# Kernel tuning notes

Hardware: AMD Instinct MI355X
Metric: run time of the kernel (lower is better)

The kernel has to match this reference:

```python
import jax, jax.numpy as jnp
import numpy as np

B, S, D, H = 8, 512, 1024, 16
DPH = D // H
MAXREL = 16
EDGE_TYPE = 4
NEG = -9e15  # matches torch's -9000000000000000.0 edge mask fill


def setup_inputs() -> dict:
    key = jax.random.key(0)
    ks = jax.random.split(key, 16)
    sd = 0.02
    inp = {
        'key':   jax.random.normal(ks[0], (B, S, D), jnp.float32),
        'value': jax.random.normal(ks[1], (B, S, D), jnp.float32),
        'query': jax.random.normal(ks[2], (B, S, D), jnp.float32),
        'grh':   jax.random.randint(ks[3], (B, S, S), 0, 5, jnp.int32),
        'mask':  jnp.zeros((B, S, S), jnp.bool_),
        # projection weights, stored (in, out)
        'Wq': jax.random.normal(ks[4], (D, D), jnp.float32) * sd,
        'bq': jnp.zeros((D,), jnp.float32),
        'Wk': jax.random.normal(ks[5], (D, D), jnp.float32) * sd,
        'bk': jnp.zeros((D,), jnp.float32),
        'Wv': jax.random.normal(ks[6], (D, D), jnp.float32) * sd,
        'bv': jnp.zeros((D,), jnp.float32),
        # relative position embedding table (vocab = 2*MAXREL+1, dph)
        'rel_emb': jax.random.normal(ks[7], (2 * MAXREL + 1, DPH), jnp.float32) * sd,
        # 2*(edge_type+1) = 10 per-head linears dph -> 1
        'att_w': jax.random.normal(ks[8], (2 * (EDGE_TYPE + 1), DPH), jnp.float32) * sd,
        'att_b': jnp.zeros((2 * (EDGE_TYPE + 1),), jnp.float32),
        # edge_type+2 = 6 gate linears D -> D
        'gate_w': jax.random.normal(ks[9], (EDGE_TYPE + 2, D, D), jnp.float32) * sd,
        'gate_b': jnp.zeros((EDGE_TYPE + 2, D), jnp.float32),
        # sub_final_linear: (D + D*edge_type) -> D
        'sub_w': jax.random.normal(ks[10], (D + D * EDGE_TYPE, D), jnp.float32) * sd,
        'sub_b': jnp.zeros((D,), jnp.float32),
    }
    return inp


def _forward(key, value, query, grh, mask, Wq, bq, Wk, bk, Wv, bv,
             rel_emb, att_w, att_b, gate_w, gate_b, sub_w, sub_b):
    def shape4(x):  # (B,S,D) -> (B,H,S,dph)
        return x.reshape(B, S, H, DPH).transpose(0, 2, 1, 3)

    def unshape(x):  # (B,H,S,dph) -> (B,S,D)
        return x.transpose(0, 2, 1, 3).reshape(B, S, D)

    q = shape4(query @ Wq + bq) / jnp.sqrt(jnp.float32(DPH))
    k = shape4(key @ Wk + bk)
    v = shape4(value @ Wv + bv)

    # relative position bias (attn_type='self', no cache)
    pos = jnp.arange(S)
    rpm = jnp.clip(pos[None, :] - pos[:, None], -MAXREL, MAXREL) + MAXREL  # (S,S)
    rel = rel_emb[rpm]  # (S,S,dph); same table used for keys and values

    scores = jnp.einsum('bhqd,bhkd->bhqk', q, k) + jnp.einsum('bhqd,qkd->bhqk', q, rel)
    scores = jnp.where(mask[:, None], jnp.float32(-1e18), scores)
    attn = jax.nn.softmax(scores, axis=-1)  # dropout p=0 (eval)

    ctx = jnp.einsum('bhqk,bhkd->bhqd', attn, v) + jnp.einsum('bhqk,qkd->bhqd', attn, rel)
    context = unshape(ctx)
    gate_context = jax.nn.sigmoid(context @ gate_w[0] + gate_b[0]) * context

    top_attn = attn[:, 0]  # (B,S,S)

    def edge_view(i0, i1, adj, gi):
        h_i = jnp.einsum('bhsd,d->bhs', v, att_w[i0]) + att_b[i0]  # (B,H,S)
        h_j = jnp.einsum('bhsd,d->bhs', v, att_w[i1]) + att_b[i1]
        e = jax.nn.leaky_relu(h_i[..., :, None] + h_j[..., None, :])  # (B,H,S,S)
        a = jax.nn.softmax(jnp.where(adj[:, None], e, jnp.float32(NEG)), axis=-1)
        sub = unshape(jnp.einsum('bhqk,bhkd->bhqd', a, v))
        return jax.nn.sigmoid(sub @ gate_w[gi] + gate_b[gi]) * sub

    # whole-graph view: adj = grh > 1, uses linear_attention[6],[7], gate_linear[-1]
    views = [edge_view(6, 7, grh > 1, EDGE_TYPE + 1)]
    eye = jnp.eye(S, dtype=grh.dtype)
    for i in range(EDGE_TYPE - 1):
        label = i + 2
        adj = grh == (label + eye * (4 - label))  # diagonal label sums to 4
        views.append(edge_view(2 * i, 2 * i + 1, adj, i + 1))

    out = jnp.concatenate([gate_context] + views, axis=-1) @ sub_w + sub_b
    return out, top_attn


def reference(key, value, query, grh, mask, Wq, bq, Wk, bk, Wv, bv,
              rel_emb, att_w, att_b, gate_w, gate_b, sub_w, sub_b):
    return _forward(key, value, query, grh, mask, Wq, bq, Wk, bk, Wv, bv,
                    rel_emb, att_w, att_b, gate_w, gate_b, sub_w, sub_b)
```

## Files before the change

### kernel.cpp

```cpp
#include <hip/hip_runtime.h>
#include <hip/hip_bf16.h>

typedef __hip_bfloat16 bf16;
typedef __attribute__((ext_vector_type(8))) short bf16x8;
typedef __attribute__((ext_vector_type(4))) float f32x4;

#define B_ 8
#define S_ 512
#define D_ 1024
#define H_ 16
#define NEGV -9.0e15f
#define WSL 1048576ull

__device__ __forceinline__ float bf2f(bf16 x) { return __bfloat162float(x); }
__device__ __forceinline__ float us2f(unsigned short u) {
  union { unsigned int i; float f; } c; c.i = ((unsigned int)u) << 16; return c.f;
}
__device__ __forceinline__ unsigned short f2us(float f) {
  bf16 h = __float2bfloat16(f);
  unsigned short u; __builtin_memcpy(&u, &h, 2); return u;
}
__device__ __forceinline__ float ldx(const void* p, size_t i, int isbf) {
  return isbf ? bf2f(((const bf16*)p)[i]) : ((const float*)p)[i];
}
struct F4 { float x, y, z, w; };
__device__ __forceinline__ F4 ld4(const void* p, size_t i, int isbf) {
  F4 r;
  if (isbf) {
    ushort4 u = *(const ushort4*)((const bf16*)p + i);
    r.x = us2f(u.x); r.y = us2f(u.y); r.z = us2f(u.z); r.w = us2f(u.w);
  } else {
    float4 d = *(const float4*)((const float*)p + i);
    r.x = d.x; r.y = d.y; r.z = d.z; r.w = d.w;
  }
  return r;
}
__device__ __forceinline__ bf16x8 ld8bf(const void* p, size_t i, int isbf) {
  if (isbf) return *(const bf16x8*)((const bf16*)p + i);
  float4 a = *(const float4*)((const float*)p + i);
  float4 b = *(const float4*)((const float*)p + i + 4);
  bf16x8 r;
  r[0] = (short)f2us(a.x); r[1] = (short)f2us(a.y);
  r[2] = (short)f2us(a.z); r[3] = (short)f2us(a.w);
  r[4] = (short)f2us(b.x); r[5] = (short)f2us(b.y);
  r[6] = (short)f2us(b.z); r[7] = (short)f2us(b.w);
  return r;
}
__device__ __forceinline__ f32x4 mfma_bf16(bf16x8 a, bf16x8 b, f32x4 c) {
  return __builtin_amdgcn_mfma_f32_16x16x32_bf16(a, b, c, 0, 0, 0);
}
__device__ __forceinline__ void gload16(const bf16* g, short* l) {
  __builtin_amdgcn_global_load_lds(
      (const __attribute__((address_space(1))) void*)g,
      (__attribute__((address_space(3))) void*)l, 16, 0, 0);
}

__global__ void detect_k(const void* __restrict__ w, int* __restrict__ flag)
{
  if (threadIdx.x == 0 && blockIdx.x == 0) {
    const unsigned short* u = (const unsigned short*)w;
    int sane = 0;
    for (int i = 0; i < 1024; i += 2) {
      float a = fabsf(us2f(u[i]));
      if (a == 0.f || (a > 9.5e-7f && a < 8.f)) sane++;
    }
    *flag = (sane > 256) ? 1 : 0;
  }
}

__global__ __launch_bounds__(256)
void cvt_k(const void* __restrict__ q, const void* __restrict__ k,
           const void* __restrict__ v, bf16* __restrict__ out,
           const int* __restrict__ dflag)
{
  const int isbf = *dflag;
  const int z = blockIdx.y;
  const void* src = z == 0 ? q : (z == 1 ? k : v);
  size_t i = ((size_t)blockIdx.x * 256 + threadIdx.x) * 8;
  bf16x8 r = ld8bf(src, i, isbf);
  *(bf16x8*)(out + (size_t)z * 4194304 + i) = r;
}

__global__ __launch_bounds__(256)
void mask_pack_k(const int* __restrict__ grh, unsigned char* __restrict__ maskp)
{
  int t = blockIdx.x * 256 + threadIdx.x;
  int byte = t & 63, qi = (t >> 6) & 511, bl = t >> 15;
  const int* g = grh + ((size_t)bl * 512 + qi) * 512 + byte * 8;
  int4 a = *(const int4*)g;
  int4 b = *(const int4*)(g + 4);
  int gs[8] = {a.x, a.y, a.z, a.w, b.x, b.y, b.z, b.w};
  unsigned int m0 = 0, m1 = 0, m2 = 0, m3 = 0;
  #pragma unroll
  for (int j = 0; j < 8; j++) {
    int k = byte * 8 + j;
    int diag = (k == qi);
    m0 |= (unsigned int)(gs[j] > 1) << j;
    m1 |= (unsigned int)(gs[j] == (diag ? 4 : 2)) << j;
    m2 |= (unsigned int)(gs[j] == (diag ? 4 : 3)) << j;
    m3 |= (unsigned int)(gs[j] == 4) << j;
  }
  size_t o = (size_t)bl * 32768 + (size_t)qi * 64 + byte;
  maskp[o]          = (unsigned char)m0;
  maskp[o + 262144] = (unsigned char)m1;
  maskp[o + 524288] = (unsigned char)m2;
  maskp[o + 786432] = (unsigned char)m3;
}

__global__ __launch_bounds__(256)
void wtrans_all_k(const void* __restrict__ Wq, const void* __restrict__ Wk,
                  const void* __restrict__ Wv, const void* __restrict__ gate_w,
                  const void* __restrict__ sub_w, bf16* __restrict__ Wt,
                  const int* __restrict__ dflag)
{
  const int isbf = *dflag;
  const int slot = blockIdx.x >> 8;
  const int blk = blockIdx.x & 255;
  const int gsrc[5] = {0, 5, 1, 2, 3};
  const void* W;
  size_t woff;
  if (slot < 3)      { W = slot == 0 ? Wq : (slot == 1 ? Wk : Wv); woff = 0; }
  else if (slot < 8) { W = gate_w; woff = (size_t)gsrc[slot - 3] * WSL; }
  else               { W = sub_w;  woff = (size_t)(slot - 8) * WSL; }
  bf16* out = Wt + (size_t)slot * WSL;

  __shared__ float t[64][68];
  const int tid = threadIdx.x;
  const int nt = blk & 15, kt = blk >> 4;
  {
    int r = tid >> 4, c4 = (tid & 15) * 4;
    #pragma unroll
    for (int i = 0; i < 4; i++) {
      int rr = r + i * 16;
      F4 v = ld4(W, woff + (size_t)(kt * 64 + rr) * 1024 + nt * 64 + c4, isbf);
      *(float4*)&t[rr][c4] = make_float4(v.x, v.y, v.z, v.w);
    }
  }
  __syncthreads();
  {
    int n = tid >> 4, k4 = (tid & 15) * 4;
    #pragma unroll
    for (int i = 0; i < 4; i++) {
      int nn = n + i * 16;
      ushort4 u;
      u.x = f2us(t[k4 + 0][nn]); u.y = f2us(t[k4 + 1][nn]);
      u.z = f2us(t[k4 + 2][nn]); u.w = f2us(t[k4 + 3][nn]);
      *(ushort4*)(out + (size_t)(nt * 64 + nn) * 1024 + kt * 64 + k4) = u;
    }
  }
}

__global__ __launch_bounds__(256)
void qkv_gemm_k(const bf16* __restrict__ qkvb, const bf16* __restrict__ Wt,
                const void* __restrict__ bqp, const void* __restrict__ bkp,
                const void* __restrict__ bvp, bf16* __restrict__ qbf,
                bf16* __restrict__ kbf, bf16* __restrict__ vtb,
                const int* __restrict__ dflag)
{
  const int isbf = *dflag;
  const int z = blockIdx.z;
  const bf16* A = qkvb + (size_t)z * 4194304;
  const void* bias = z == 0 ? bqp : (z == 1 ? bkp : bvp);
  bf16* outB = z == 0 ? qbf : (z == 1 ? kbf : vtb);
  const bf16* Wz = Wt + (size_t)z * WSL;
  const float scale = z == 0 ? 0.125f : 1.0f;
  const int vtrans = (z == 2);

  __shared__ short As[128 * 64];
  __shared__ short Bs[128 * 64];
  const int tid = threadIdx.x;
  const int w = tid >> 6, ln = tid & 63;
  const int ln15 = ln & 15, quad = ln >> 4;
  const int wm = (w & 1) * 64, wn = (w >> 1) * 64;
  const int bm = blockIdx.x * 128, bn = blockIdx.y * 128;
  const int rbase = w * 8 + (ln >> 3);
  const int goff = ((ln & 7) ^ (ln >> 3)) * 8;
  f32x4 acc[4][4];
  #pragma unroll
  for (int mt = 0; mt < 4; mt++)
    #pragma unroll
    for (int nt = 0; nt < 4; nt++) acc[mt][nt] = (f32x4)(0.0f);

  for (int k0 = 0; k0 < 1024; k0 += 64) {
    #pragma unroll
    for (int i = 0; i < 4; i++) {
      int r = i * 32 + rbase;
      gload16(A + (size_t)(bm + r) * 1024 + k0 + goff,
              &As[(i * 32 + w * 8) * 64]);
      gload16(Wz + (size_t)(bn + r) * 1024 + k0 + goff,
              &Bs[(i * 32 + w * 8) * 64]);
    }
    __syncthreads();
    #pragma unroll
    for (int s = 0; s < 2; s++) {
      bf16x8 af[4], bfr[4];
      #pragma unroll
      for (int t = 0; t < 4; t++) {
        int ra = wm + t * 16 + ln15;
        af[t] = *(bf16x8*)&As[ra * 64 + (((s * 4 + quad) ^ (ra & 7)) * 8)];
        int rb = wn + t * 16 + ln15;
        bfr[t] = *(bf16x8*)&Bs[rb * 64 + (((s * 4 + quad) ^ (rb & 7)) * 8)];
      }
      #pragma unroll
      for (int mt = 0; mt < 4; mt++)
        #pragma unroll
        for (int nt = 0; nt < 4; nt++)
          acc[mt][nt] = mfma_bf16(af[mt], bfr[nt], acc[mt][nt]);
    }
    __syncthreads();
  }

  #pragma unroll
  for (int nt = 0; nt < 4; nt++) {
    int col = bn + wn + nt * 16 + ln15;
    float bv = ldx(bias, col, isbf);
    #pragma unroll
    for (int mt = 0; mt < 4; mt++) {
      #pragma unroll
      for (int r = 0; r < 4; r++) {
        int row = bm + wm + mt * 16 + quad * 4 + r;
        float v = (acc[mt][nt][r] + bv) * scale;
        int bb = row >> 9, s = row & 511;
        int h = col >> 6, d0 = col & 63;
        size_t o = vtrans ? (((size_t)(bb * 16 + h) * 64 + d0) * 512 + s)
                          : (((size_t)(bb * 16 + h) * 512 + s) * 64 + d0);
        outB[o] = __float2bfloat16(v);
      }
    }
  }
}

__global__ __launch_bounds__(256)
void gate_gemm_k(const bf16* __restrict__ ctx5, const bf16* __restrict__ Wt,
                 const void* __restrict__ gate_b, bf16* __restrict__ gated5,
                 const int* __restrict__ dflag)
{
  const int isbf = *dflag;
  const int z = blockIdx.z;
  const int gsel[5] = {0, 5, 1, 2, 3};
  const bf16* A = ctx5 + (size_t)z * 4194304;
  bf16* outB = gated5 + (size_t)z * 4194304;
  const bf16* Wz = Wt + (size_t)(3 + z) * WSL;
  const size_t boff = (size_t)gsel[z] * 1024;

  __shared__ short As[128 * 64];
  __shared__ short Bs[128 * 64];
  const int tid = threadIdx.x;
  const int w = tid >> 6, ln = tid & 63;
  const int ln15 = ln & 15, quad = ln >> 4;
  const int wm = (w & 1) * 64, wn = (w >> 1) * 64;
  const int bm = blockIdx.x * 128, bn = blockIdx.y * 128;
  const int rbase = w * 8 + (ln >> 3);
  const int goff = ((ln & 7) ^ (ln >> 3)) * 8;
  f32x4 acc[4][4];
  #pragma unroll
  for (int mt = 0; mt < 4; mt++)
    #pragma unroll
    for (int nt = 0; nt < 4; nt++) acc[mt][nt] = (f32x4)(0.0f);

  for (int k0 = 0; k0 < 1024; k0 += 64) {
    #pragma unroll
    for (int i = 0; i < 4; i++) {
      int r = i * 32 + rbase;
      gload16(A + (size_t)(bm + r) * 1024 + k0 + goff,
              &As[(i * 32 + w * 8) * 64]);
      gload16(Wz + (size_t)(bn + r) * 1024 + k0 + goff,
              &Bs[(i * 32 + w * 8) * 64]);
    }
    __syncthreads();
    #pragma unroll
    for (int s = 0; s < 2; s++) {
      bf16x8 af[4], bfr[4];
      #pragma unroll
      for (int t = 0; t < 4; t++) {
        int ra = wm + t * 16 + ln15;
        af[t] = *(bf16x8*)&As[ra * 64 + (((s * 4 + quad) ^ (ra & 7)) * 8)];
        int rb = wn + t * 16 + ln15;
        bfr[t] = *(bf16x8*)&Bs[rb * 64 + (((s * 4 + quad) ^ (rb & 7)) * 8)];
      }
      #pragma unroll
      for (int mt = 0; mt < 4; mt++)
        #pragma unroll
        for (int nt = 0; nt < 4; nt++)
          acc[mt][nt] = mfma_bf16(af[mt], bfr[nt], acc[mt][nt]);
    }
    __syncthreads();
  }

  #pragma unroll
  for (int nt = 0; nt < 4; nt++) {
    int col = bn + wn + nt * 16 + ln15;
    float bv = ldx(gate_b, boff + col, isbf);
    #pragma unroll
    for (int mt = 0; mt < 4; mt++) {
      #pragma unroll
      for (int r = 0; r < 4; r++) {
        int row = bm + wm + mt * 16 + quad * 4 + r;
        float v = acc[mt][nt][r] + bv;
        float x = bf2f(A[(size_t)row * 1024 + col]);
        outB[(size_t)row * 1024 + col] = __float2bfloat16(x / (1.f + __expf(-v)));
      }
    }
  }
}

__global__ __launch_bounds__(256)
void sub_gemm_k(const bf16* __restrict__ gated5, const bf16* __restrict__ Wt,
                const void* __restrict__ sub_b, void* __restrict__ dout,
                const int* __restrict__ dflag)
{
  const int isbf = *dflag;
  __shared__ short As[128 * 64];
  __shared__ short Bs[128 * 64];
  const int tid = threadIdx.x;
  const int w = tid >> 6, ln = tid & 63;
  const int ln15 = ln & 15, quad = ln >> 4;
  const int wm = (w & 1) * 64, wn = (w >> 1) * 64;
  const int bm = blockIdx.x * 128, bn = blockIdx.y * 128;
  const int rbase = w * 8 + (ln >> 3);
  const int goff = ((ln & 7) ^ (ln >> 3)) * 8;
  f32x4 acc[4][4];
  #pragma unroll
  for (int mt = 0; mt < 4; mt++)
    #pragma unroll
    for (int nt = 0; nt < 4; nt++) acc[mt][nt] = (f32x4)(0.0f);

  for (int k0 = 0; k0 < 5120; k0 += 64) {
    const int slot = k0 >> 10, kk = k0 & 1023;
    const bf16* Ab = gated5 + (size_t)slot * 4194304;
    const bf16* Wz = Wt + (size_t)(8 + slot) * WSL;
    #pragma unroll
    for (int i = 0; i < 4; i++) {
      int r = i * 32 + rbase;
      gload16(Ab + (size_t)(bm + r) * 1024 + kk + goff,
              &As[(i * 32 + w * 8) * 64]);
      gload16(Wz + (size_t)(bn + r) * 1024 + kk + goff,
              &Bs[(i * 32 + w * 8) * 64]);
    }
    __syncthreads();
    #pragma unroll
    for (int s = 0; s < 2; s++) {
      bf16x8 af[4], bfr[4];
      #pragma unroll
      for (int t = 0; t < 4; t++) {
        int ra = wm + t * 16 + ln15;
        af[t] = *(bf16x8*)&As[ra * 64 + (((s * 4 + quad) ^ (ra & 7)) * 8)];
        int rb = wn + t * 16 + ln15;
        bfr[t] = *(bf16x8*)&Bs[rb * 64 + (((s * 4 + quad) ^ (rb & 7)) * 8)];
      }
      #pragma unroll
      for (int mt = 0; mt < 4; mt++)
        #pragma unroll
        for (int nt = 0; nt < 4; nt++)
          acc[mt][nt] = mfma_bf16(af[mt], bfr[nt], acc[mt][nt]);
    }
    __syncthreads();
  }

  #pragma unroll
  for (int nt = 0; nt < 4; nt++) {
    int col = bn + wn + nt * 16 + ln15;
    float bv = ldx(sub_b, col, isbf);
    #pragma unroll
    for (int mt = 0; mt < 4; mt++) {
      #pragma unroll
      for (int r = 0; r < 4; r++) {
        int row = bm + wm + mt * 16 + quad * 4 + r;
        float v = acc[mt][nt][r] + bv;
        size_t o = (size_t)row * 1024 + col;
        if (isbf) ((bf16*)dout)[o] = __float2bfloat16(v);
        else      ((float*)dout)[o] = v;
      }
    }
  }
}

__global__ __launch_bounds__(256)
void qrel_k(const bf16* __restrict__ qbf, const void* __restrict__ rel_emb,
            float* __restrict__ G, const int* __restrict__ dflag)
{
  const int isbf = *dflag;
  __shared__ float rel[33][65];
  __shared__ float qw[4][64];
  const int tid = threadIdx.x;
  for (int i = tid; i < 33 * 64; i += 256)
    rel[i >> 6][i & 63] = ldx(rel_emb, i, isbf);
  const int wv = tid >> 6, lane = tid & 63;
  const size_t row = (size_t)blockIdx.x * 4 + wv;
  qw[wv][lane] = bf2f(qbf[row * 64 + lane]);
  __syncthreads();
  if (lane < 33) {
    float s = 0.f;
    #pragma unroll
    for (int d = 0; d < 64; d++) s += qw[wv][d] * rel[lane][d];
    G[row * 33 + lane] = s;
  }
}

__global__ __launch_bounds__(256, 2)
void score_fused_k(const bf16* __restrict__ qbf, const bf16* __restrict__ kbf,
                   const float* __restrict__ G, const bf16* __restrict__ vt,
                   const void* __restrict__ rel_emb, bf16* __restrict__ ctx,
                   void* __restrict__ dout, const int* __restrict__ dflag)
{
  __shared__ short P[32 * 512];
  __shared__ float gbuf[32 * 33];
  __shared__ float relbuf[33 * 64];
  __shared__ float smax[4][16];
  __shared__ float ssumS[4][16];
  __shared__ float sleS[4][16];
  __shared__ float sgeS[4][16];
  const int tid = threadIdx.x;
  const int w = tid >> 6, ln = tid & 63;
  const int ln15 = ln & 15, quad = ln >> 4;
  const int rowg = (w >> 1) * 16;
  const int ch = w & 1;
  const int bh = blockIdx.x, qt = blockIdx.y;
  const size_t qrow0 = (size_t)bh * 512 + qt * 32;
  const int isbf = *dflag;

  for (int i = tid; i < 32 * 33; i += 256) {
    int r = i / 33, c = i - r * 33;
    gbuf[i] = G[(qrow0 + r) * 33 + c];
  }
  for (int i = tid; i < 33 * 64; i += 256)
    relbuf[i] = ldx(rel_emb, i, isbf);

  const bf16* qrow = qbf + (qrow0 + rowg + ln15) * 64;
  bf16x8 af0 = *(const bf16x8*)(qrow + quad * 8);
  bf16x8 af1 = *(const bf16x8*)(qrow + 32 + quad * 8);
  const bf16* kb = kbf + (size_t)bh * 512 * 64;
  f32x4 acc[16];
  #pragma unroll
  for (int t = 0; t < 16; t++) acc[t] = (f32x4)(0.0f);
  #pragma unroll
  for (int t = 0; t < 16; t++) {
    const bf16* kr = kb + (size_t)(ch * 256 + t * 16 + ln15) * 64 + quad * 8;
    bf16x8 b0 = *(const bf16x8*)kr;
    bf16x8 b1 = *(const bf16x8*)(kr + 32);
    acc[t] = mfma_bf16(af0, b0, acc[t]);
    acc[t] = mfma_bf16(af1, b1, acc[t]);
  }
  __syncthreads();

  const int qg = qt * 32 + rowg + quad * 4;
  const int rowl0 = rowg + quad * 4;
  float mx[4], ssum[4], sle[4], sge[4], inv[4];
  #pragma unroll
  for (int r = 0; r < 4; r++) mx[r] = -3.0e38f;
  #pragma unroll
  for (int t = 0; t < 16; t++) {
    int k = ch * 256 + t * 16 + ln15;
    #pragma unroll
    for (int r = 0; r < 4; r++) {
      int delta = k - (qg + r);
      int bkt = delta < -16 ? 0 : (delta > 16 ? 32 : delta + 16);
      float s = acc[t][r] + gbuf[(rowl0 + r) * 33 + bkt];
      acc[t][r] = s;
      mx[r] = fmaxf(mx[r], s);
    }
  }
  #pragma unroll
  for (int r = 0; r < 4; r++) {
    float m = mx[r];
    #pragma unroll
    for (int off = 1; off < 16; off <<= 1) m = fmaxf(m, __shfl_xor(m, off));
    mx[r] = m;
  }
  if (ln15 == 0) {
    #pragma unroll
    for (int r = 0; r < 4; r++) smax[w][quad * 4 + r] = mx[r];
  }
  __syncthreads();
  #pragma unroll
  for (int r = 0; r < 4; r++) {
    mx[r] = fmaxf(mx[r], smax[w ^ 1][quad * 4 + r]);
    ssum[r] = 0.f; sle[r] = 0.f; sge[r] = 0.f;
  }

  #pragma unroll
  for (int t = 0; t < 16; t++) {
    int k = ch * 256 + t * 16 + ln15;
    #pragma unroll
    for (int r = 0; r < 4; r++) {
      float p = __expf(acc[t][r] - mx[r]);
      acc[t][r] = p;
      ssum[r] += p;
      int delta = k - (qg + r);
      if (delta <= -16) sle[r] += p;
      if (delta >= 16) sge[r] += p;
    }
  }
  #pragma unroll
  for (int r = 0; r < 4; r++) {
    #pragma unroll
    for (int off = 1; off < 16; off <<= 1) {
      ssum[r] += __shfl_xor(ssum[r], off);
      sle[r] += __shfl_xor(sle[r], off);
      sge[r] += __shfl_xor(sge[r], off);
    }
  }
  if (ln15 == 0) {
    #pragma unroll
    for (int r = 0; r < 4; r++) {
      ssumS[w][quad * 4 + r] = ssum[r];
      sleS[w][quad * 4 + r] = sle[r];
      sgeS[w][quad * 4 + r] = sge[r];
    }
  }
  __syncthreads();
  #pragma unroll
  for (int r = 0; r < 4; r++) {
    float tot = ssum[r] + ssumS[w ^ 1][quad * 4 + r];
    sle[r] += sleS[w ^ 1][quad * 4 + r];
    sge[r] += sgeS[w ^ 1][quad * 4 + r];
    inv[r] = 1.f / tot;
  }

  #pragma unroll
  for (int t2 = 0; t2 < 16; t2++) {
    int gg = t2 * 2 + (ln15 >> 3);
    int slot = gg ^ (quad << 1);
    #pragma unroll
    for (int r = 0; r < 4; r++) {
      int rowL = rowl0 + r;
      P[rowL * 512 + ch * 256 + slot * 8 + (ln15 & 7)] =
          (short)f2us(acc[t2][r] * inv[r]);
    }
  }
  __syncthreads();

  if ((bh & 15) == 0) {
    const int bg = bh >> 4;
    for (int i = tid; i < 32 * 64; i += 256) {
      int rowL = i >> 6, g = i & 63;
      int chg = g >> 5, gg = g & 31;
      int slot = gg ^ (((rowL >> 2) & 3) << 1);
      bf16x8 u = *(bf16x8*)&P[rowL * 512 + chg * 256 + slot * 8];
      size_t o = (size_t)4194304 + (size_t)bg * 262144 +
                 (size_t)(qt * 32 + rowL) * 512 + g * 8;
      if (isbf) {
        *(bf16x8*)((bf16*)dout + o) = u;
      } else {
        float4 f0 = make_float4(us2f((unsigned short)u[0]), us2f((unsigned short)u[1]),
                                us2f((unsigned short)u[2]), us2f((unsigned short)u[3]));
        float4 f1 = make_float4(us2f((unsigned short)u[4]), us2f((unsigned short)u[5]),
                                us2f((unsigned short)u[6]), us2f((unsigned short)u[7]));
        *(float4*)((float*)dout + o) = f0;
        *(float4*)((float*)dout + o + 4) = f1;
      }
    }
  }

  const bf16* vb = vt + (size_t)bh * 64 * 512;
  f32x4 pacc[2];
  pacc[0] = (f32x4)(0.0f); pacc[1] = (f32x4)(0.0f);
  const int ra = rowg + ln15;
  const int rsw = ((ln15 >> 2) & 3) << 1;
  #pragma unroll
  for (int h2 = 0; h2 < 2; h2++) {
    #pragma unroll
    for (int kk = 0; kk < 8; kk++) {
      int gg = kk * 4 + quad;
      bf16x8 a = *(bf16x8*)&P[ra * 512 + h2 * 256 + ((gg ^ rsw) * 8)];
      int k0 = h2 * 256 + kk * 32;
      #pragma unroll
      for (int nt2 = 0; nt2 < 2; nt2++) {
        int dcol = ch * 32 + nt2 * 16 + ln15;
        bf16x8 b = *(const bf16x8*)(vb + (size_t)dcol * 512 + k0 + quad * 8);
        pacc[nt2] = mfma_bf16(a, b, pacc[nt2]);
      }
    }
  }

  for (int rr = 1; rr < 32; rr++) {
    float av[4];
    #pragma unroll
    for (int r = 0; r < 4; r++) {
      int k = qg + r + rr - 16;
      av[r] = 0.f;
      if (k >= 0 && k < 512) {
        int g = k >> 3, chg = g >> 5, gg = g & 31;
        int slot = gg ^ (quad << 1);
        av[r] = us2f((unsigned short)P[(rowl0 + r) * 512 + chg * 256 +
                                       slot * 8 + (k & 7)]);
      }
    }
    #pragma unroll
    for (int nt2 = 0; nt2 < 2; nt2++) {
      float relv = relbuf[rr * 64 + ch * 32 + nt2 * 16 + ln15];
      #pragma unroll
      for (int r = 0; r < 4; r++) pacc[nt2][r] += av[r] * relv;
    }
  }

  #pragma unroll
  for (int nt2 = 0; nt2 < 2; nt2++) {
    float r0v = relbuf[ch * 32 + nt2 * 16 + ln15];
    float r32v = relbuf[32 * 64 + ch * 32 + nt2 * 16 + ln15];
    #pragma unroll
    for (int r = 0; r < 4; r++)
      pacc[nt2][r] += sle[r] * inv[r] * r0v + sge[r] * inv[r] * r32v;
  }

  const int bl = bh >> 4, head = bh & 15;
  #pragma unroll
  for (int r = 0; r < 4; r++) {
    int s = qt * 32 + rowl0 + r;
    #pragma unroll
    for (int nt2 = 0; nt2 < 2; nt2++)
      ctx[((size_t)bl * 512 + s) * 1024 + head * 64 + ch * 32 + nt2 * 16 + ln15] =
          __float2bfloat16(pacc[nt2][r]);
  }
}

__global__ __launch_bounds__(256)
void hv_k(const bf16* __restrict__ vt, const void* __restrict__ att_w,
          const void* __restrict__ att_b, float* __restrict__ h0,
          float* __restrict__ h1, const int* __restrict__ dflag)
{
  const int i0s[4] = {6, 0, 2, 4};
  const int i1s[4] = {7, 1, 3, 5};
  const int z = blockIdx.y;
  const int i0 = i0s[z], i1 = i1s[z];
  __shared__ float w0[64], w1[64];
  const int tid = threadIdx.x;
  const int bh = blockIdx.x;
  const int isbf = *dflag;
  if (tid < 64) {
    w0[tid] = ldx(att_w, i0 * 64 + tid, isbf);
    w1[tid] = ldx(att_w, i1 * 64 + tid, isbf);
  }
  __syncthreads();
  const bf16* vb = vt + (size_t)bh * 64 * 512 + tid * 2;
  float a00 = 0, a01 = 0, a10 = 0, a11 = 0;
  for (int d = 0; d < 64; d++) {
    ushort2 u = *(const ushort2*)(vb + (size_t)d * 512);
    float f0 = us2f(u.x), f1 = us2f(u.y);
    a00 += f0 * w0[d]; a10 += f1 * w0[d];
    a01 += f0 * w1[d]; a11 += f1 * w1[d];
  }
  float b0 = ldx(att_b, i0, isbf), b1 = ldx(att_b, i1, isbf);
  float* p0 = h0 + (size_t)z * 65536 + (size_t)bh * 512 + tid * 2;
  float* p1 = h1 + (size_t)z * 65536 + (size_t)bh * 512 + tid * 2;
  p0[0] = a00 + b0; p0[1] = a10 + b0;
  p1[0] = a01 + b1; p1[1] = a11 + b1;
}

__global__ __launch_bounds__(256)
void edge_fused_k(const float* __restrict__ h0, const float* __restrict__ h1,
                  const unsigned char* __restrict__ maskp,
                  const bf16* __restrict__ vt, bf16* __restrict__ ctx5)
{
  __shared__ short P[32 * 512];
  const int tid = threadIdx.x;
  const int w = tid >> 6, ln = tid & 63;
  const int ln15 = ln & 15, quad = ln >> 4;
  const int bh = blockIdx.x, qt = blockIdx.y, view = blockIdx.z;
  const int bl = bh >> 4;
  bf16* ctx = ctx5 + (size_t)(1 + view) * 4194304;

  {
    const float* hjp = h1 + (size_t)view * 65536 + (size_t)bh * 512 + ln * 8;
    float4 hA = *(const float4*)hjp;
    float4 hB = *(const float4*)(hjp + 4);
    float hjv[8] = {hA.x, hA.y, hA.z, hA.w, hB.x, hB.y, hB.z, hB.w};
    const float* h0b = h0 + (size_t)view * 65536 + (size_t)bh * 512 + qt * 32 + w * 8;
    const unsigned char* mrow = maskp + (size_t)view * 262144 + (size_t)bl * 32768
                                + (size_t)(qt * 32 + w * 8) * 64 + ln;
    unsigned int mb[8];
    float hi[8];
    #pragma unroll
    for (int rr = 0; rr < 8; rr++) mb[rr] = mrow[rr * 64];
    #pragma unroll
    for (int rr = 0; rr < 8; rr++) hi[rr] = h0b[rr];

    float e[8][8];
    float mx[8], sm[8];
    #pragma unroll
    for (int rr = 0; rr < 8; rr++) {
      float m = -3.0e38f;
      #pragma unroll
      for (int j = 0; j < 8; j++) {
        float ej = hi[rr] + hjv[j];
        ej = ej >= 0.f ? ej : 0.01f * ej;
        e[rr][j] = ((mb[rr] >> j) & 1) ? ej : NEGV;
        m = fmaxf(m, e[rr][j]);
      }
      mx[rr] = m;
    }
    #pragma unroll
    for (int off = 32; off; off >>= 1) {
      #pragma unroll
      for (int rr = 0; rr < 8; rr++)
        mx[rr] = fmaxf(mx[rr], __shfl_xor(mx[rr], off));
    }
    #pragma unroll
    for (int rr = 0; rr < 8; rr++) {
      float s = 0.f;
      #pragma unroll
      for (int j = 0; j < 8; j++) {
        e[rr][j] = __expf(e[rr][j] - mx[rr]);
        s += e[rr][j];
      }
      sm[rr] = s;
    }
    #pragma unroll
    for (int off = 32; off; off >>= 1) {
      #pragma unroll
      for (int rr = 0; rr < 8; rr++)
        sm[rr] += __shfl_xor(sm[rr], off);
    }
    #pragma unroll
    for (int rr = 0; rr < 8; rr++) {
      float inv = 1.f / sm[rr];
      int r = w * 8 + rr;
      bf16x8 pv;
      #pragma unroll
      for (int j = 0; j < 8; j++) pv[j] = (short)f2us(e[rr][j] * inv);
      *(bf16x8*)&P[r * 512 + ((ln ^ (r & 7)) * 8)] = pv;
    }
  }
  __syncthreads();

  const bf16* vb = vt + (size_t)bh * 64 * 512;
  const int m0 = (w >> 1) * 16, d0 = (w & 1) * 32;
  f32x4 acc[2];
  acc[0] = (f32x4)(0.0f); acc[1] = (f32x4)(0.0f);

  const int ra = m0 + ln15;
  const int rsw = ra & 7;
  #pragma unroll 4
  for (int k0 = 0; k0 < 512; k0 += 32) {
    int gsel = (k0 >> 3) + quad;
    bf16x8 a = *(bf16x8*)&P[ra * 512 + ((gsel ^ rsw) * 8)];
    #pragma unroll
    for (int nt = 0; nt < 2; nt++) {
      bf16x8 b = *(const bf16x8*)(vb + (size_t)(d0 + nt * 16 + ln15) * 512 + k0 + quad * 8);
      acc[nt] = mfma_bf16(a, b, acc[nt]);
    }
  }

  const int head = bh & 15;
  #pragma unroll
  for (int r = 0; r < 4; r++) {
    int s = qt * 32 + m0 + quad * 4 + r;
    #pragma unroll
    for (int nt = 0; nt < 2; nt++)
      ctx[((size_t)bl * 512 + s) * 1024 + head * 64 + d0 + nt * 16 + ln15] =
          __float2bfloat16(acc[nt][r]);
  }
}

extern "C" void kernel_launch(void* const* d_in, const int* in_sizes, int n_in,
                              void* d_out, int out_size, void* d_ws, size_t ws_size,
                              hipStream_t stream)
{
  const void* key   = d_in[0];
  const void* value = d_in[1];
  const void* query = d_in[2];
  const int*  grh   = (const int*)d_in[3];
  const void* Wq = d_in[5];
  const void* bq = d_in[6];
  const void* Wk = d_in[7];
  const void* bk = d_in[8];
  const void* Wv = d_in[9];
  const void* bv = d_in[10];
  const void* rel_emb = d_in[11];
  const void* att_w = d_in[12];
  const void* att_b = d_in[13];
  const void* gate_w = d_in[14];
  const void* gate_b = d_in[15];
  const void* sub_w = d_in[16];
  const void* sub_b = d_in[17];

  int* dflag = (int*)d_ws;
  float* base = (float*)d_ws;
  bf16* qbf = (bf16*)(base + 16);
  bf16* kbf = (bf16*)(base + 16 + 2097152);
  bf16* vtb = (bf16*)(base + 16 + 2 * 2097152);
  bf16* Wt  = (bf16*)(base + 16 + 3 * 2097152);
  float* G  = base + 16 + 3 * 2097152 + 6815744;
  float* h0 = G + 2162688;
  float* h1 = h0 + 262144;
  bf16* ctx5   = (bf16*)(h1 + 262144);
  bf16* gated5 = ctx5 + 5ull * 4194304;
  unsigned char* maskp = (unsigned char*)(gated5 + 5ull * 4194304);
  bf16* qkvb = (bf16*)(maskp + 1048576);

  detect_k<<<dim3(1), dim3(64), 0, stream>>>(Wq, dflag);

  mask_pack_k<<<dim3(1024), dim3(256), 0, stream>>>(grh, maskp);

  cvt_k<<<dim3(2048, 3), dim3(256), 0, stream>>>(query, key, value, qkvb, dflag);

  wtrans_all_k<<<dim3(13 * 256), dim3(256), 0, stream>>>(
      Wq, Wk, Wv, gate_w, sub_w, Wt, dflag);

  qkv_gemm_k<<<dim3(32, 8, 3), dim3(256), 0, stream>>>(
      qkvb, Wt, bq, bk, bv, qbf, kbf, vtb, dflag);

  qrel_k<<<dim3(16384), dim3(256), 0, stream>>>(qbf, rel_emb, G, dflag);

  score_fused_k<<<dim3(128, 16), dim3(256), 0, stream>>>(
      qbf, kbf, G, vtb, rel_emb, ctx5, d_out, dflag);

  hv_k<<<dim3(128, 4), dim3(256), 0, stream>>>(vtb, att_w, att_b, h0, h1, dflag);
  edge_fused_k<<<dim3(128, 16, 4), dim3(256), 0, stream>>>(
      h0, h1, maskp, vtb, ctx5);

  gate_gemm_k<<<dim3(32, 8, 5), dim3(256), 0, stream>>>(
      ctx5, Wt, gate_b, gated5, dflag);
  sub_gemm_k<<<dim3(32, 8), dim3(256), 0, stream>>>(
      gated5, Wt, sub_b, d_out, dflag);
}
```

Measured before the change: 753.4 us.

## Merge prep kernels and interleave score and edge attention in one launch

Combines the input conversion, weight transpose and mask packing kernels into a single prep launch that dispatches on block index. It also merges the score and edge attention kernels into one launch that interleaves score and edge blocks (1 score per 4 edge blocks) over a shared LDS buffer, with hv_k moved ahead of it. The aim is to cut launch overhead and tail gaps between kernels and to let the heavier score blocks overlap with edge blocks on the device. The merged kernel sizes its shared memory for the larger score path and runs under launch_bounds(256,2), which may lower occupancy for the edge blocks.

```diff
diff --git a/kernel.cpp b/kernel.cpp
--- a/kernel.cpp
+++ b/kernel.cpp
@@ -69,84 +69,80 @@
 }
 
 __global__ __launch_bounds__(256)
-void cvt_k(const void* __restrict__ q, const void* __restrict__ k,
-           const void* __restrict__ v, bf16* __restrict__ out,
-           const int* __restrict__ dflag)
-{
-  const int isbf = *dflag;
-  const int z = blockIdx.y;
-  const void* src = z == 0 ? q : (z == 1 ? k : v);
-  size_t i = ((size_t)blockIdx.x * 256 + threadIdx.x) * 8;
-  bf16x8 r = ld8bf(src, i, isbf);
-  *(bf16x8*)(out + (size_t)z * 4194304 + i) = r;
-}
-
-__global__ __launch_bounds__(256)
-void mask_pack_k(const int* __restrict__ grh, unsigned char* __restrict__ maskp)
-{
-  int t = blockIdx.x * 256 + threadIdx.x;
-  int byte = t & 63, qi = (t >> 6) & 511, bl = t >> 15;
-  const int* g = grh + ((size_t)bl * 512 + qi) * 512 + byte * 8;
-  int4 a = *(const int4*)g;
-  int4 b = *(const int4*)(g + 4);
-  int gs[8] = {a.x, a.y, a.z, a.w, b.x, b.y, b.z, b.w};
-  unsigned int m0 = 0, m1 = 0, m2 = 0, m3 = 0;
-  #pragma unroll
-  for (int j = 0; j < 8; j++) {
-    int k = byte * 8 + j;
-    int diag = (k == qi);
-    m0 |= (unsigned int)(gs[j] > 1) << j;
-    m1 |= (unsigned int)(gs[j] == (diag ? 4 : 2)) << j;
-    m2 |= (unsigned int)(gs[j] == (diag ? 4 : 3)) << j;
-    m3 |= (unsigned int)(gs[j] == 4) << j;
-  }
-  size_t o = (size_t)bl * 32768 + (size_t)qi * 64 + byte;
-  maskp[o]          = (unsigned char)m0;
-  maskp[o + 262144] = (unsigned char)m1;
-  maskp[o + 524288] = (unsigned char)m2;
-  maskp[o + 786432] = (unsigned char)m3;
-}
-
-__global__ __launch_bounds__(256)
-void wtrans_all_k(const void* __restrict__ Wq, const void* __restrict__ Wk,
-                  const void* __restrict__ Wv, const void* __restrict__ gate_w,
-                  const void* __restrict__ sub_w, bf16* __restrict__ Wt,
-                  const int* __restrict__ dflag)
-{
-  const int isbf = *dflag;
-  const int slot = blockIdx.x >> 8;
-  const int blk = blockIdx.x & 255;
-  const int gsrc[5] = {0, 5, 1, 2, 3};
-  const void* W;
-  size_t woff;
-  if (slot < 3)      { W = slot == 0 ? Wq : (slot == 1 ? Wk : Wv); woff = 0; }
-  else if (slot < 8) { W = gate_w; woff = (size_t)gsrc[slot - 3] * WSL; }
-  else               { W = sub_w;  woff = (size_t)(slot - 8) * WSL; }
-  bf16* out = Wt + (size_t)slot * WSL;
-
+void prep_k(const void* __restrict__ q, const void* __restrict__ k,
+            const void* __restrict__ v, bf16* __restrict__ qkvb,
+            const int* __restrict__ grh, unsigned char* __restrict__ maskp,
+            const void* __restrict__ Wq, const void* __restrict__ Wk,
+            const void* __restrict__ Wv, const void* __restrict__ gate_w,
+            const void* __restrict__ sub_w, bf16* __restrict__ Wt,
+            const int* __restrict__ dflag)
+{
+  const int bid = blockIdx.x;
+  const int tid = threadIdx.x;
   __shared__ float t[64][68];
-  const int tid = threadIdx.x;
-  const int nt = blk & 15, kt = blk >> 4;
-  {
-    int r = tid >> 4, c4 = (tid & 15) * 4;
-    #pragma unroll
-    for (int i = 0; i < 4; i++) {
-      int rr = r + i * 16;
-      F4 v = ld4(W, woff + (size_t)(kt * 64 + rr) * 1024 + nt * 64 + c4, isbf);
-      *(float4*)&t[rr][c4] = make_float4(v.x, v.y, v.z, v.w);
-    }
-  }
-  __syncthreads();
-  {
-    int n = tid >> 4, k4 = (tid & 15) * 4;
-    #pragma unroll
-    for (int i = 0; i < 4; i++) {
-      int nn = n + i * 16;
-      ushort4 u;
-      u.x = f2us(t[k4 + 0][nn]); u.y = f2us(t[k4 + 1][nn]);
-      u.z = f2us(t[k4 + 2][nn]); u.w = f2us(t[k4 + 3][nn]);
-      *(ushort4*)(out + (size_t)(nt * 64 + nn) * 1024 + kt * 64 + k4) = u;
-    }
+  if (bid < 6144) {
+    const int isbf = *dflag;
+    const int z = bid >> 11, blk = bid & 2047;
+    const void* src = z == 0 ? q : (z == 1 ? k : v);
+    size_t i = ((size_t)blk * 256 + tid) * 8;
+    bf16x8 r = ld8bf(src, i, isbf);
+    *(bf16x8*)(qkvb + (size_t)z * 4194304 + i) = r;
+  } else if (bid < 9472) {
+    const int isbf = *dflag;
+    const int tt = bid - 6144;
+    const int slot = tt >> 8;
+    const int blk = tt & 255;
+    const int gsrc[5] = {0, 5, 1, 2, 3};
+    const void* W;
+    size_t woff;
+    if (slot < 3)      { W = slot == 0 ? Wq : (slot == 1 ? Wk : Wv); woff = 0; }
+    else if (slot < 8) { W = gate_w; woff = (size_t)gsrc[slot - 3] * WSL; }
+    else               { W = sub_w;  woff = (size_t)(slot - 8) * WSL; }
+    bf16* out = Wt + (size_t)slot * WSL;
+    const int nt = blk & 15, kt = blk >> 4;
+    {
+      int r = tid >> 4, c4 = (tid & 15) * 4;
+      #pragma unroll
+      for (int i = 0; i < 4; i++) {
+        int rr = r + i * 16;
+        F4 vv = ld4(W, woff + (size_t)(kt * 64 + rr) * 1024 + nt * 64 + c4, isbf);
+        *(float4*)&t[rr][c4] = make_float4(vv.x, vv.y, vv.z, vv.w);
+      }
+    }
+    __syncthreads();
+    {
+      int n = tid >> 4, k4 = (tid & 15) * 4;
+      #pragma unroll
+      for (int i = 0; i < 4; i++) {
+        int nn = n + i * 16;
+        ushort4 u;
+        u.x = f2us(t[k4 + 0][nn]); u.y = f2us(t[k4 + 1][nn]);
+        u.z = f2us(t[k4 + 2][nn]); u.w = f2us(t[k4 + 3][nn]);
+        *(ushort4*)(out + (size_t)(nt * 64 + nn) * 1024 + kt * 64 + k4) = u;
+      }
+    }
+  } else {
+    int tfl = (bid - 9472) * 256 + tid;
+    int byte = tfl & 63, qi = (tfl >> 6) & 511, bl = tfl >> 15;
+    const int* g = grh + ((size_t)bl * 512 + qi) * 512 + byte * 8;
+    int4 a = *(const int4*)g;
+    int4 b = *(const int4*)(g + 4);
+    int gs[8] = {a.x, a.y, a.z, a.w, b.x, b.y, b.z, b.w};
+    unsigned int m0 = 0, m1 = 0, m2 = 0, m3 = 0;
+    #pragma unroll
+    for (int j = 0; j < 8; j++) {
+      int kk = byte * 8 + j;
+      int diag = (kk == qi);
+      m0 |= (unsigned int)(gs[j] > 1) << j;
+      m1 |= (unsigned int)(gs[j] == (diag ? 4 : 2)) << j;
+      m2 |= (unsigned int)(gs[j] == (diag ? 4 : 3)) << j;
+      m3 |= (unsigned int)(gs[j] == 4) << j;
+    }
+    size_t o = (size_t)bl * 32768 + (size_t)qi * 64 + byte;
+    maskp[o]          = (unsigned char)m0;
+    maskp[o + 262144] = (unsigned char)m1;
+    maskp[o + 524288] = (unsigned char)m2;
+    maskp[o + 786432] = (unsigned char)m3;
   }
 }
 
@@ -397,25 +393,60 @@
   }
 }
 
-__global__ __launch_bounds__(256, 2)
-void score_fused_k(const bf16* __restrict__ qbf, const bf16* __restrict__ kbf,
-                   const float* __restrict__ G, const bf16* __restrict__ vt,
-                   const void* __restrict__ rel_emb, bf16* __restrict__ ctx,
-                   void* __restrict__ dout, const int* __restrict__ dflag)
-{
-  __shared__ short P[32 * 512];
-  __shared__ float gbuf[32 * 33];
-  __shared__ float relbuf[33 * 64];
-  __shared__ float smax[4][16];
-  __shared__ float ssumS[4][16];
-  __shared__ float sleS[4][16];
-  __shared__ float sgeS[4][16];
+__global__ __launch_bounds__(256)
+void hv_k(const bf16* __restrict__ vt, const void* __restrict__ att_w,
+          const void* __restrict__ att_b, float* __restrict__ h0,
+          float* __restrict__ h1, const int* __restrict__ dflag)
+{
+  const int i0s[4] = {6, 0, 2, 4};
+  const int i1s[4] = {7, 1, 3, 5};
+  const int z = blockIdx.y;
+  const int i0 = i0s[z], i1 = i1s[z];
+  __shared__ float w0[64], w1[64];
+  const int tid = threadIdx.x;
+  const int bh = blockIdx.x;
+  const int isbf = *dflag;
+  if (tid < 64) {
+    w0[tid] = ldx(att_w, i0 * 64 + tid, isbf);
+    w1[tid] = ldx(att_w, i1 * 64 + tid, isbf);
+  }
+  __syncthreads();
+  const bf16* vb = vt + (size_t)bh * 64 * 512 + tid * 2;
+  float a00 = 0, a01 = 0, a10 = 0, a11 = 0;
+  for (int d = 0; d < 64; d++) {
+    ushort2 u = *(const ushort2*)(vb + (size_t)d * 512);
+    float f0 = us2f(u.x), f1 = us2f(u.y);
+    a00 += f0 * w0[d]; a10 += f1 * w0[d];
+    a01 += f0 * w1[d]; a11 += f1 * w1[d];
+  }
+  float b0 = ldx(att_b, i0, isbf), b1 = ldx(att_b, i1, isbf);
+  float* p0 = h0 + (size_t)z * 65536 + (size_t)bh * 512 + tid * 2;
+  float* p1 = h1 + (size_t)z * 65536 + (size_t)bh * 512 + tid * 2;
+  p0[0] = a00 + b0; p0[1] = a10 + b0;
+  p1[0] = a01 + b1; p1[1] = a11 + b1;
+}
+
+__device__ void score_body(char* smem, int bh, int qt,
+                           const bf16* __restrict__ qbf,
+                           const bf16* __restrict__ kbf,
+                           const float* __restrict__ G,
+                           const bf16* __restrict__ vt,
+                           const void* __restrict__ rel_emb,
+                           bf16* __restrict__ ctx, void* __restrict__ dout,
+                           const int* __restrict__ dflag)
+{
+  short* P = (short*)smem;
+  float* gbuf = (float*)(smem + 32768);
+  float* relbuf = (float*)(smem + 36992);
+  float (*smax)[16]  = (float(*)[16])(smem + 45440);
+  float (*ssumS)[16] = (float(*)[16])(smem + 45696);
+  float (*sleS)[16]  = (float(*)[16])(smem + 45952);
+  float (*sgeS)[16]  = (float(*)[16])(smem + 46208);
   const int tid = threadIdx.x;
   const int w = tid >> 6, ln = tid & 63;
   const int ln15 = ln & 15, quad = ln >> 4;
   const int rowg = (w >> 1) * 16;
   const int ch = w & 1;
-  const int bh = blockIdx.x, qt = blockIdx.y;
   const size_t qrow0 = (size_t)bh * 512 + qt * 32;
   const int isbf = *dflag;
 
@@ -614,49 +645,17 @@
   }
 }
 
-__global__ __launch_bounds__(256)
-void hv_k(const bf16* __restrict__ vt, const void* __restrict__ att_w,
-          const void* __restrict__ att_b, float* __restrict__ h0,
-          float* __restrict__ h1, const int* __restrict__ dflag)
-{
-  const int i0s[4] = {6, 0, 2, 4};
-  const int i1s[4] = {7, 1, 3, 5};
-  const int z = blockIdx.y;
-  const int i0 = i0s[z], i1 = i1s[z];
-  __shared__ float w0[64], w1[64];
-  const int tid = threadIdx.x;
-  const int bh = blockIdx.x;
-  const int isbf = *dflag;
-  if (tid < 64) {
-    w0[tid] = ldx(att_w, i0 * 64 + tid, isbf);
-    w1[tid] = ldx(att_w, i1 * 64 + tid, isbf);
-  }
-  __syncthreads();
-  const bf16* vb = vt + (size_t)bh * 64 * 512 + tid * 2;
-  float a00 = 0, a01 = 0, a10 = 0, a11 = 0;
-  for (int d = 0; d < 64; d++) {
-    ushort2 u = *(const ushort2*)(vb + (size_t)d * 512);
-    float f0 = us2f(u.x), f1 = us2f(u.y);
-    a00 += f0 * w0[d]; a10 += f1 * w0[d];
-    a01 += f0 * w1[d]; a11 += f1 * w1[d];
-  }
-  float b0 = ldx(att_b, i0, isbf), b1 = ldx(att_b, i1, isbf);
-  float* p0 = h0 + (size_t)z * 65536 + (size_t)bh * 512 + tid * 2;
-  float* p1 = h1 + (size_t)z * 65536 + (size_t)bh * 512 + tid * 2;
-  p0[0] = a00 + b0; p0[1] = a10 + b0;
-  p1[0] = a01 + b1; p1[1] = a11 + b1;
-}
-
-__global__ __launch_bounds__(256)
-void edge_fused_k(const float* __restrict__ h0, const float* __restrict__ h1,
-                  const unsigned char* __restrict__ maskp,
-                  const bf16* __restrict__ vt, bf16* __restrict__ ctx5)
-{
-  __shared__ short P[32 * 512];
+__device__ void edge_body(char* smem, int bh, int qt, int view,
+                          const float* __restrict__ h0,
+                          const float* __restrict__ h1,
+                          const unsigned char* __restrict__ maskp,
+                          const bf16* __restrict__ vt,
+                          bf16* __restrict__ ctx5)
+{
+  short* P = (short*)smem;
   const int tid = threadIdx.x;
   const int w = tid >> 6, ln = tid & 63;
   const int ln15 = ln & 15, quad = ln >> 4;
-  const int bh = blockIdx.x, qt = blockIdx.y, view = blockIdx.z;
   const int bl = bh >> 4;
   bf16* ctx = ctx5 + (size_t)(1 + view) * 4194304;
 
@@ -749,6 +748,26 @@
     for (int nt = 0; nt < 2; nt++)
       ctx[((size_t)bl * 512 + s) * 1024 + head * 64 + d0 + nt * 16 + ln15] =
           __float2bfloat16(acc[nt][r]);
+  }
+}
+
+__global__ __launch_bounds__(256, 2)
+void attn_merged_k(const bf16* __restrict__ qbf, const bf16* __restrict__ kbf,
+                   const float* __restrict__ G, const bf16* __restrict__ vt,
+                   const void* __restrict__ rel_emb, bf16* __restrict__ ctx5,
+                   void* __restrict__ dout, const int* __restrict__ dflag,
+                   const float* __restrict__ h0, const float* __restrict__ h1,
+                   const unsigned char* __restrict__ maskp)
+{
+  __shared__ __align__(16) char smem[46464];
+  const int bid = blockIdx.x;
+  const int g = bid / 5, r = bid % 5;
+  if (r == 0) {
+    score_body(smem, g & 127, g >> 7, qbf, kbf, G, vt, rel_emb, ctx5, dout, dflag);
+  } else {
+    int e = g * 4 + (r - 1);
+    int rem = e & 2047;
+    edge_body(smem, rem & 127, rem >> 7, e >> 11, h0, h1, maskp, vt, ctx5);
   }
 }
 
@@ -790,24 +809,17 @@
 
   detect_k<<<dim3(1), dim3(64), 0, stream>>>(Wq, dflag);
 
-  mask_pack_k<<<dim3(1024), dim3(256), 0, stream>>>(grh, maskp);
-
-  cvt_k<<<dim3(2048, 3), dim3(256), 0, stream>>>(query, key, value, qkvb, dflag);
-
-  wtrans_all_k<<<dim3(13 * 256), dim3(256), 0, stream>>>(
-      Wq, Wk, Wv, gate_w, sub_w, Wt, dflag);
+  prep_k<<<dim3(10496), dim3(256), 0, stream>>>(
+      query, key, value, qkvb, grh, maskp, Wq, Wk, Wv, gate_w, sub_w, Wt, dflag);
 
   qkv_gemm_k<<<dim3(32, 8, 3), dim3(256), 0, stream>>>(
       qkvb, Wt, bq, bk, bv, qbf, kbf, vtb, dflag);
 
   qrel_k<<<dim3(16384), dim3(256), 0, stream>>>(qbf, rel_emb, G, dflag);
-
-  score_fused_k<<<dim3(128, 16), dim3(256), 0, stream>>>(
-      qbf, kbf, G, vtb, rel_emb, ctx5, d_out, dflag);
-
   hv_k<<<dim3(128, 4), dim3(256), 0, stream>>>(vtb, att_w, att_b, h0, h1, dflag);
-  edge_fused_k<<<dim3(128, 16, 4), dim3(256), 0, stream>>>(
-      h0, h1, maskp, vtb, ctx5);
+
+  attn_merged_k<<<dim3(10240), dim3(256), 0, stream>>>(
+      qbf, kbf, G, vtb, rel_emb, ctx5, d_out, dflag, h0, h1, maskp);
 
   gate_gemm_k<<<dim3(32, 8, 5), dim3(256), 0, stream>>>(
       ctx5, Wt, gate_b, gated5, dflag);
```

New measurement: 793.4 us. 1.05x slower.
